# Optimization experiments

Hardware: AMD Instinct MI355X
Metric: run time of the kernel (lower is better)

The kernel has to match this reference:

```python
import jax, jax.numpy as jnp
import numpy as np

NUM_IMAGE_PATCHES = 4096
HIDDEN = 1536
NUM_HEADS = 12
HEAD_DIM = HIDDEN // NUM_HEADS  # 128
MLP_HIDDEN = 4 * HIDDEN  # 6144
TXT_LEN = 256
L_X = TXT_LEN + NUM_IMAGE_PATCHES  # 4352
NUM_CONCEPTS = 20
L_C = NUM_CONCEPTS + NUM_IMAGE_PATCHES  # 4116


def setup_inputs() -> dict:
    key = jax.random.key(0)
    ks = jax.random.split(key, 10)
    B = 1
    f = lambda k, s, sc=1.0: jax.random.normal(k, s, dtype=jnp.float32) * sc
    return {
        "x": f(ks[0], (B, L_X, HIDDEN)),
        "concepts": f(ks[1], (B, NUM_CONCEPTS, HIDDEN)),
        "vec": f(ks[2], (B, HIDDEN)),
        "pe": f(ks[3], (1, 1, L_X, HEAD_DIM // 2, 2, 2)),
        "concept_pe": f(ks[4], (1, 1, L_C, HEAD_DIM // 2, 2, 2)),
        # linear1: hidden -> 3*hidden + mlp_hidden (torch Linear: y = x @ W.T + b)
        "w1": f(ks[5], (3 * HIDDEN + MLP_HIDDEN, HIDDEN), 0.02),
        "b1": jnp.zeros((3 * HIDDEN + MLP_HIDDEN,), jnp.float32),
        # linear2: hidden + mlp_hidden -> hidden
        "w2": f(ks[6], (HIDDEN, HIDDEN + MLP_HIDDEN), 0.02),
        "b2": jnp.zeros((HIDDEN,), jnp.float32),
        # QKNorm learned RMSNorm scales (per head_dim)
        "q_scale": jnp.ones((HEAD_DIM,), jnp.float32),
        "k_scale": jnp.ones((HEAD_DIM,), jnp.float32),
        # Modulation(double=False): silu(vec) -> 3*hidden (shift, scale, gate)
        "mod_w": f(ks[7], (3 * HIDDEN, HIDDEN), 0.02),
        "mod_b": jnp.zeros((3 * HIDDEN,), jnp.float32),
    }


def _layernorm(x):  # elementwise_affine=False, eps=1e-6
    mu = x.mean(-1, keepdims=True)
    var = ((x - mu) ** 2).mean(-1, keepdims=True)
    return (x - mu) * jax.lax.rsqrt(var + 1e-6)


def _rmsnorm(x, scale):  # FLUX RMSNorm with learned scale
    return x * jax.lax.rsqrt((x * x).mean(-1, keepdims=True) + 1e-6) * scale


def _apply_rope(t, pe):
    # t: [B,H,L,D]; pe: [1,1,L,D/2,2,2]
    ts = t.reshape(*t.shape[:-1], -1, 1, 2)  # [B,H,L,D/2,1,2]
    out = pe[..., 0] * ts[..., 0] + pe[..., 1] * ts[..., 1]  # [B,H,L,D/2,2]
    return out.reshape(t.shape)


def _attention(q, k, v, pe):
    q = _apply_rope(q, pe)
    k = _apply_rope(k, pe)
    scale = jnp.asarray(1.0 / np.sqrt(q.shape[-1]), q.dtype)
    logits = jnp.einsum("bhqd,bhkd->bhqk", q, k) * scale
    a = jax.nn.softmax(logits, axis=-1)
    o = jnp.einsum("bhqk,bhkd->bhqd", a, v)
    B, H, L, D = o.shape
    return o.transpose(0, 2, 1, 3).reshape(B, L, H * D)  # B L (H D)


def reference(x, concepts, vec, pe, concept_pe, w1, b1, w2, b2,
              q_scale, k_scale, mod_w, mod_b):
    H = HIDDEN
    # Modulation: lin(silu(vec))[:, None].chunk(3) -> shift, scale, gate
    m = jax.nn.silu(vec) @ mod_w.T + mod_b
    shift, scale, gate = [t[:, None, :] for t in jnp.split(m, 3, axis=-1)]

    def block(inp, pe_in):
        xm = (1.0 + scale) * _layernorm(inp) + shift
        h = xm @ w1.T + b1
        qkv, mlp = h[..., : 3 * H], h[..., 3 * H:]
        B, L = inp.shape[0], inp.shape[1]
        # 'B L (K H D) -> K B H L D'
        qkv = qkv.reshape(B, L, 3, NUM_HEADS, HEAD_DIM).transpose(2, 0, 3, 1, 4)
        q, k, v = qkv[0], qkv[1], qkv[2]
        q = _rmsnorm(q, q_scale)
        k = _rmsnorm(k, k_scale)
        attn = _attention(q, k, v, pe_in)
        return jnp.concatenate([attn, jax.nn.gelu(mlp, approximate=True)], axis=2) @ w2.T + b2

    output = block(x, pe)

    img = x[:, -NUM_IMAGE_PATCHES:]
    img_concept_x = jnp.concatenate([concepts, img], axis=1)
    output_img_concept = block(img_concept_x, concept_pe)
    concept_output = output_img_concept[:, :-NUM_IMAGE_PATCHES]

    return (x + gate * output, concepts + gate * concept_output)
```

## Files before the change

kernel.cpp:

```cpp
#include <hip/hip_runtime.h>
#include <cstdint>
#include <cstddef>

typedef float        f32x4  __attribute__((ext_vector_type(4)));
typedef __bf16       bf16x8 __attribute__((ext_vector_type(8)));
typedef unsigned int u32x4  __attribute__((ext_vector_type(4)));
typedef unsigned int u32x2  __attribute__((ext_vector_type(2)));

static constexpr int HID   = 1536;
static constexpr int NHEAD = 12;
static constexpr int HD    = 128;
static constexpr int NQKV  = 10752;
static constexpr int CATK  = 7680;
static constexpr int LX    = 4352;
static constexpr int LC2   = 4116;
static constexpr int NCON  = 20;

static constexpr float QSCL = 0.08838834764831845f * 1.4426950408889634f;
static constexpr float SHIFT = 24.0f;

static constexpr size_t OFF_MVEC = 0;
static constexpr size_t OFF_W1B  = 18432;
static constexpr size_t OFF_W2B  = OFF_W1B  + 33030144ull;
static constexpr size_t OFF_XM1  = OFF_W2B  + 23592960ull;
static constexpr size_t OFF_QH1  = OFF_XM1;
static constexpr size_t OFF_QKV1 = OFF_XM1  + 13369344ull;
static constexpr size_t OFF_KH1  = OFF_QKV1 + 26738688ull;
static constexpr size_t OFF_VH1  = OFF_KH1  + 13369344ull;
static constexpr size_t OFF_CAT1 = OFF_VH1  + 13369344ull;
static constexpr size_t OFF_XM2  = OFF_CAT1;
static constexpr size_t OFF_QKV2 = OFF_XM2  + 196608ull;
static constexpr size_t OFF_VH2S = OFF_QKV2 + 196608ull;
static constexpr size_t OFF_QH2  = OFF_VH2S + 98304ull;
static constexpr size_t OFF_KH2  = OFF_QH2  + 196608ull;
static constexpr size_t OFF_CAT2 = OFF_KH2  + 12644352ull;

__device__ __forceinline__ void gload_lds16(const void* g, void* l)
{
  __builtin_amdgcn_global_load_lds(
      (const __attribute__((address_space(1))) unsigned int*)g,
      (__attribute__((address_space(3))) unsigned int*)l, 16, 0, 0);
}

#define PHASE_BAR() asm volatile("s_barrier" ::: "memory")


__global__ __launch_bounds__(256) void f2b_kernel(const float* __restrict__ in,
                                                  __bf16* __restrict__ out, int n4)
{
  int i = blockIdx.x * 256 + threadIdx.x;
  if (i >= n4) return;
  f32x4 v = *((const f32x4*)in + i);
  union { __bf16 h[4]; u32x2 u; } cv;
  cv.h[0] = (__bf16)v[0]; cv.h[1] = (__bf16)v[1];
  cv.h[2] = (__bf16)v[2]; cv.h[3] = (__bf16)v[3];
  *((u32x2*)out + i) = cv.u;
}

__global__ __launch_bounds__(256) void mod_kernel(const float* __restrict__ vec,
                                                  const float* __restrict__ mod_w,
                                                  const float* __restrict__ mod_b,
                                                  float* __restrict__ m)
{
  int o = blockIdx.x * 4 + (threadIdx.x >> 6);
  int lane = threadIdx.x & 63;
  float s = 0.0f;
  for (int k = lane; k < HID; k += 64) {
    float v = vec[k];
    float sv = v / (1.0f + expf(-v));
    s += sv * mod_w[(size_t)o * HID + k];
  }
  #pragma unroll
  for (int msk = 32; msk; msk >>= 1) s += __shfl_xor(s, msk);
  if (lane == 0) m[o] = s + mod_b[o];
}

__device__ __forceinline__ float block_sum256(float v, float* red)
{
  #pragma unroll
  for (int msk = 32; msk; msk >>= 1) v += __shfl_xor(v, msk);
  int w = threadIdx.x >> 6;
  if ((threadIdx.x & 63) == 0) red[w] = v;
  __syncthreads();
  float s = red[0] + red[1] + red[2] + red[3];
  __syncthreads();
  return s;
}

__global__ __launch_bounds__(256) void ln_mod_kernel(const float* __restrict__ x,
                                                     const float* __restrict__ mvec,
                                                     __bf16* __restrict__ out)
{
  __shared__ float red[4];
  size_t row = blockIdx.x;
  const float* xr = x + row * HID;
  float v[6]; float s = 0.0f;
  #pragma unroll
  for (int i = 0; i < 6; i++) { v[i] = xr[threadIdx.x + i * 256]; s += v[i]; }
  float mu = block_sum256(s, red) * (1.0f / HID);
  float s2 = 0.0f;
  #pragma unroll
  for (int i = 0; i < 6; i++) { float d = v[i] - mu; s2 += d * d; }
  float var = block_sum256(s2, red) * (1.0f / HID);
  float rinv = rsqrtf(var + 1e-6f);
  #pragma unroll
  for (int i = 0; i < 6; i++) {
    int h = threadIdx.x + i * 256;
    float xm = (v[i] - mu) * rinv;
    xm = (1.0f + mvec[HID + h]) * xm + mvec[h];
    out[row * HID + h] = (__bf16)xm;
  }
}

template<int MODE>
__global__ __launch_bounds__(512, 2) void gemm256(const __bf16* __restrict__ A,
                                                  const __bf16* __restrict__ B,
                                                  int M, int K,
                                                  const float* __restrict__ bias,
                                                  __bf16* __restrict__ qkv_out,
                                                  __bf16* __restrict__ cat_out,
                                                  __bf16* __restrict__ vh_out, int vkeys,
                                                  const float* __restrict__ res,
                                                  const float* __restrict__ gate,
                                                  float* __restrict__ out)
{
  const int tid = threadIdx.x;
  const int lane = tid & 63, wave = tid >> 6;
  const int quad = lane >> 4, l16 = lane & 15;
  const int wmh = wave >> 2;
  const int wnq = wave & 3;
  const int m0 = blockIdx.y * 256, n0 = blockIdx.x * 256;
  const int swz = (l16 & 4) ? 16 : 0;

  __shared__ __bf16 As[2][256][64];
  __shared__ __bf16 Bs[2][256][64];

  const f32x4 fzero = {0.0f, 0.0f, 0.0f, 0.0f};
  f32x4 acc[8][4];
  #pragma unroll
  for (int i = 0; i < 8; i++)
    #pragma unroll
    for (int j = 0; j < 4; j++) acc[i][j] = fzero;

  const int srow = lane >> 3;
  const int scol = ((lane & 7) * 8) ^ ((lane & 32) ? 16 : 0);
  const __bf16* Ag = A + (size_t)(m0 + wave * 32 + srow) * K + scol;
  const __bf16* Bg = B + (size_t)(n0 + wave * 32 + srow) * K + scol;

  auto stageA = [&](int buf, int k) {
    #pragma unroll
    for (int j = 0; j < 4; j++)
      gload_lds16(Ag + (size_t)(j * 8) * K + k, &As[buf][wave * 32 + j * 8][0]);
  };
  auto stageB = [&](int buf, int k) {
    #pragma unroll
    for (int j = 0; j < 4; j++)
      gload_lds16(Bg + (size_t)(j * 8) * K + k, &Bs[buf][wave * 32 + j * 8][0]);
  };

  const int NT = K >> 6;
  stageB(0, 0);  stageA(0, 0);
  stageB(1, 64); stageA(1, 64);
  asm volatile("s_waitcnt vmcnt(8)" ::: "memory");
  PHASE_BAR();

  for (int t = 0; t < NT; ++t) {
    const int b = t & 1;
    const int kn = (t + 2) << 6;
    bf16x8 aM[4][2], bN0[2][2], bN1[2][2];

    #pragma unroll
    for (int f = 0; f < 4; f++)
      #pragma unroll
      for (int kk = 0; kk < 2; kk++)
        aM[f][kk] = *(const bf16x8*)&As[b][wmh * 128 + f * 16 + l16][(kk * 32 + quad * 8) ^ swz];
    #pragma unroll
    for (int g = 0; g < 2; g++)
      #pragma unroll
      for (int kk = 0; kk < 2; kk++)
        bN0[g][kk] = *(const bf16x8*)&Bs[b][wnq * 64 + g * 16 + l16][(kk * 32 + quad * 8) ^ swz];
    PHASE_BAR();
    __builtin_amdgcn_s_setprio(1);
    #pragma unroll
    for (int f = 0; f < 4; f++)
      #pragma unroll
      for (int g = 0; g < 2; g++)
        #pragma unroll
        for (int kk = 0; kk < 2; kk++)
          acc[f][g] = __builtin_amdgcn_mfma_f32_16x16x32_bf16(aM[f][kk], bN0[g][kk], acc[f][g], 0, 0, 0);
    __builtin_amdgcn_s_setprio(0);
    PHASE_BAR();

    #pragma unroll
    for (int g = 0; g < 2; g++)
      #pragma unroll
      for (int kk = 0; kk < 2; kk++)
        bN1[g][kk] = *(const bf16x8*)&Bs[b][wnq * 64 + 32 + g * 16 + l16][(kk * 32 + quad * 8) ^ swz];
    PHASE_BAR();
    __builtin_amdgcn_s_setprio(1);
    #pragma unroll
    for (int f = 0; f < 4; f++)
      #pragma unroll
      for (int g = 0; g < 2; g++)
        #pragma unroll
        for (int kk = 0; kk < 2; kk++)
          acc[f][2 + g] = __builtin_amdgcn_mfma_f32_16x16x32_bf16(aM[f][kk], bN1[g][kk], acc[f][2 + g], 0, 0, 0);
    __builtin_amdgcn_s_setprio(0);
    PHASE_BAR();

    #pragma unroll
    for (int f = 0; f < 4; f++)
      #pragma unroll
      for (int kk = 0; kk < 2; kk++)
        aM[f][kk] = *(const bf16x8*)&As[b][wmh * 128 + 64 + f * 16 + l16][(kk * 32 + quad * 8) ^ swz];
    if (t + 2 < NT) stageB(b, kn);
    PHASE_BAR();
    __builtin_amdgcn_s_setprio(1);
    #pragma unroll
    for (int f = 0; f < 4; f++)
      #pragma unroll
      for (int g = 0; g < 2; g++)
        #pragma unroll
        for (int kk = 0; kk < 2; kk++)
          acc[4 + f][2 + g] = __builtin_amdgcn_mfma_f32_16x16x32_bf16(aM[f][kk], bN1[g][kk], acc[4 + f][2 + g], 0, 0, 0);
    __builtin_amdgcn_s_setprio(0);
    PHASE_BAR();

    if (t + 2 < NT) stageA(b, kn);
    PHASE_BAR();
    __builtin_amdgcn_s_setprio(1);
    #pragma unroll
    for (int f = 0; f < 4; f++)
      #pragma unroll
      for (int g = 0; g < 2; g++)
        #pragma unroll
        for (int kk = 0; kk < 2; kk++)
          acc[4 + f][g] = __builtin_amdgcn_mfma_f32_16x16x32_bf16(aM[f][kk], bN0[g][kk], acc[4 + f][g], 0, 0, 0);
    __builtin_amdgcn_s_setprio(0);
    if (t + 1 < NT) {
      if (t + 2 < NT) asm volatile("s_waitcnt vmcnt(8)" ::: "memory");
      else            asm volatile("s_waitcnt vmcnt(0)" ::: "memory");
    }
    PHASE_BAR();
  }

  #pragma unroll
  for (int mf = 0; mf < 8; mf++) {
    #pragma unroll
    for (int r = 0; r < 4; r++) {
      int gm = m0 + wmh * 128 + mf * 16 + quad * 4 + r;
      if (gm >= M) continue;
      #pragma unroll
      for (int nf = 0; nf < 4; nf++) {
        int gn = n0 + wnq * 64 + nf * 16 + l16;
        float v = acc[mf][nf][r] + bias[gn];
        if constexpr (MODE == 0) {
          if (gn < 3072) {
            qkv_out[(size_t)gm * 3072 + gn] = (__bf16)v;
          } else if (gn < 4608) {
            vh_out[(size_t)(gn - 3072) * vkeys + gm] = (__bf16)v;
          } else {
            float g = 0.5f * v * (1.0f + tanhf(0.7978845608028654f * (v + 0.044715f * v * v * v)));
            cat_out[(size_t)gm * CATK + (gn - 3072)] = (__bf16)g;
          }
        } else {
          out[(size_t)gm * HID + gn] = res[(size_t)gm * HID + gn] + gate[gn] * v;
        }
      }
    }
  }
}

template<int MODE>
__global__ __launch_bounds__(256) void gemm_bt(const __bf16* __restrict__ A,
                                               const __bf16* __restrict__ B,
                                               int M, int K,
                                               const float* __restrict__ bias,
                                               __bf16* __restrict__ qkv_out,
                                               __bf16* __restrict__ cat_out,
                                               __bf16* __restrict__ vh_out, int vkeys,
                                               const float* __restrict__ res,
                                               const float* __restrict__ gate,
                                               float* __restrict__ out)
{
  const int tid = threadIdx.x;
  const int lane = tid & 63, wave = tid >> 6;
  const int quad = lane >> 4, l16 = lane & 15;
  const int m0 = blockIdx.y * 128, n0 = blockIdx.x * 128;
  const int wm = (wave & 1) * 64, wn = (wave >> 1) * 64;

  __shared__ __bf16 As[128][64];
  __shared__ __bf16 Bs[128][64];

  const f32x4 fzero = {0.0f, 0.0f, 0.0f, 0.0f};
  f32x4 acc[4][4];
  #pragma unroll
  for (int i = 0; i < 4; i++)
    #pragma unroll
    for (int j = 0; j < 4; j++) acc[i][j] = fzero;

  const int srow = lane >> 3;
  const int scol = (lane & 7) * 8;
  const int rbase = wave * 32 + srow;
  const __bf16* Ab = A + (size_t)(m0 + rbase) * K + scol;
  const __bf16* Bb = B + (size_t)(n0 + rbase) * K + scol;

  for (int k0 = 0; k0 < K; k0 += 64) {
    __syncthreads();
    #pragma unroll
    for (int j = 0; j < 4; j++) {
      gload_lds16(Ab + (size_t)(j * 8) * K + k0, &As[wave * 32 + j * 8][0]);
      gload_lds16(Bb + (size_t)(j * 8) * K + k0, &Bs[wave * 32 + j * 8][0]);
    }
    __syncthreads();
    #pragma unroll
    for (int kk = 0; kk < 64; kk += 32) {
      bf16x8 af[4], bfr[4];
      #pragma unroll
      for (int i = 0; i < 4; i++) af[i]  = *(const bf16x8*)&As[wm + i * 16 + l16][kk + quad * 8];
      #pragma unroll
      for (int j = 0; j < 4; j++) bfr[j] = *(const bf16x8*)&Bs[wn + j * 16 + l16][kk + quad * 8];
      #pragma unroll
      for (int i = 0; i < 4; i++)
        #pragma unroll
        for (int j = 0; j < 4; j++)
          acc[i][j] = __builtin_amdgcn_mfma_f32_16x16x32_bf16(af[i], bfr[j], acc[i][j], 0, 0, 0);
    }
  }

  #pragma unroll
  for (int i = 0; i < 4; i++) {
    #pragma unroll
    for (int r = 0; r < 4; r++) {
      int gm = m0 + wm + i * 16 + quad * 4 + r;
      if (gm >= M) continue;
      #pragma unroll
      for (int j = 0; j < 4; j++) {
        int gn = n0 + wn + j * 16 + l16;
        float v = acc[i][j][r] + bias[gn];
        if constexpr (MODE == 0) {
          if (gn < 3072) {
            qkv_out[(size_t)gm * 3072 + gn] = (__bf16)v;
          } else if (gn < 4608) {
            vh_out[(size_t)(gn - 3072) * vkeys + gm] = (__bf16)v;
          } else {
            float g = 0.5f * v * (1.0f + tanhf(0.7978845608028654f * (v + 0.044715f * v * v * v)));
            cat_out[(size_t)gm * CATK + (gn - 3072)] = (__bf16)g;
          }
        } else {
          out[(size_t)gm * HID + gn] = res[(size_t)gm * HID + gn] + gate[gn] * v;
        }
      }
    }
  }
}

__global__ __launch_bounds__(256) void qk_prep(const __bf16* __restrict__ src0, int rows0,
                                               const __bf16* __restrict__ src1, int off1,
                                               int total_rows, int q_rows,
                                               const float* __restrict__ pe,
                                               const float* __restrict__ qscale,
                                               const float* __restrict__ kscale,
                                               __bf16* __restrict__ qh, int q_stride,
                                               __bf16* __restrict__ kh, int k_stride)
{
  int wid = blockIdx.x * 4 + (threadIdx.x >> 6);
  int lane = threadIdx.x & 63;
  int r = wid / NHEAD, h = wid - (wid / NHEAD) * NHEAD;
  if (r >= total_rows) return;
  const __bf16* src = (r < rows0) ? (src0 + (size_t)r * 3072)
                                  : (src1 + (size_t)(r + off1) * 3072);
  const float* pep = pe + ((size_t)r * 64 + lane) * 4;
  float e00 = pep[0], e01 = pep[1], e10 = pep[2], e11 = pep[3];

  {
    const __bf16* p = src + HID + h * HD + 2 * lane;
    float a = (float)p[0], b = (float)p[1];
    float ss = a * a + b * b;
    #pragma unroll
    for (int msk = 32; msk; msk >>= 1) ss += __shfl_xor(ss, msk);
    float rinv = rsqrtf(ss * (1.0f / HD) + 1e-6f);
    a *= rinv * kscale[2 * lane]; b *= rinv * kscale[2 * lane + 1];
    float ra = e00 * a + e01 * b, rb = e10 * a + e11 * b;
    __bf16* o = kh + ((size_t)h * k_stride + r) * HD + 2 * lane;
    o[0] = (__bf16)ra; o[1] = (__bf16)rb;
  }
  if (r < q_rows) {
    const __bf16* p = src + h * HD + 2 * lane;
    float a = (float)p[0], b = (float)p[1];
    float ss = a * a + b * b;
    #pragma unroll
    for (int msk = 32; msk; msk >>= 1) ss += __shfl_xor(ss, msk);
    float rinv = rsqrtf(ss * (1.0f / HD) + 1e-6f);
    a *= rinv * qscale[2 * lane]; b *= rinv * qscale[2 * lane + 1];
    float ra = (e00 * a + e01 * b) * QSCL, rb = (e10 * a + e11 * b) * QSCL;
    __bf16* o = qh + ((size_t)h * q_stride + r) * HD + 2 * lane;
    o[0] = (__bf16)ra; o[1] = (__bf16)rb;
  }
}

template<int GEN>
__global__ __launch_bounds__(512, 4) void attn_kernel(const __bf16* __restrict__ qh,
                                                      const __bf16* __restrict__ kh,
                                                      const __bf16* __restrict__ vA, int vA_stride,
                                                      const __bf16* __restrict__ vB, int vB_stride,
                                                      int v_boff, int v_split,
                                                      int Lq, int Lk, int q_stride, int k_stride,
                                                      int nqt,
                                                      __bf16* __restrict__ cat_out)
{
  const int tid = threadIdx.x, lane = tid & 63, wave = tid >> 6;
  const int quad = lane >> 4, l16 = lane & 15;
  const int qsub = wave >> 1, kg = wave & 1;

  int bid = blockIdx.x;
  if constexpr (GEN == 0) {
    int nb = gridDim.x;
    if ((nb & 7) == 0) {
      int per = nb >> 3;
      bid = (bid & 7) * per + (bid >> 3);
    }
  }
  const int head = bid / nqt, qt = bid - head * nqt;
  const int q0 = qt * 64 + qsub * 16;

  __shared__ __align__(16) unsigned char lds_raw[46080];
  __bf16 (*Ks)[136]     = (__bf16(*)[136])(lds_raw);
  __bf16 (*Vt)[72]      = (__bf16(*)[72])(lds_raw + 17408);
  __bf16 (*Ps)[16][40]  = (__bf16(*)[16][40])(lds_raw + 35840);
  float*  Of            = (float*)lds_raw;
  float*  Lf            = (float*)(lds_raw + 35840);

  const f32x4 fzero = {0.0f, 0.0f, 0.0f, 0.0f};
  const u32x4 uzero = {0, 0, 0, 0};

  bf16x8 ones;
  #pragma unroll
  for (int e = 0; e < 8; e++) ones[e] = (__bf16)1.0f;

  bf16x8 qf[4];
  {
    int qrow = q0 + l16;
    if (GEN == 0 || qrow < Lq) {
      const __bf16* qp = qh + ((size_t)head * q_stride + qrow) * HD + quad * 8;
      #pragma unroll
      for (int c = 0; c < 4; c++) qf[c] = *(const bf16x8*)(qp + c * 32);
    } else {
      #pragma unroll
      for (int c = 0; c < 4; c++) qf[c] = __builtin_bit_cast(bf16x8, uzero);
    }
  }
  f32x4 o[8];
  #pragma unroll
  for (int d = 0; d < 8; d++) o[d] = fzero;
  f32x4 l_acc = fzero;

  const int krowA = tid >> 4, kcolA = (tid & 15) * 8;
  const int vdimA = tid >> 3, vkcA  = tid & 7;

  const __bf16* khb = kh + (size_t)head * k_stride * HD;
  const __bf16* vaB = vA + (size_t)head * HD * vA_stride;
  const __bf16* vbB = vB + (size_t)head * HD * vB_stride + v_boff;

  auto vload = [&](int dim, int kb) -> u32x4 {
    if constexpr (GEN == 0) {
      return *(const u32x4*)(vbB + (size_t)dim * vB_stride + kb);
    } else {
      u32x4 vd = uzero;
      if (kb < Lk) {
        if (kb + 8 <= v_split) {
          vd = *(const u32x4*)(vaB + (size_t)dim * vA_stride + kb);
        } else if (kb >= v_split && kb + 8 <= Lk) {
          vd = *(const u32x4*)(vbB + (size_t)dim * vB_stride + kb);
        } else {
          __bf16* ve = (__bf16*)&vd;
          #pragma unroll
          for (int e = 0; e < 8; e++) {
            int key = kb + e;
            if (key < Lk)
              ve[e] = (key < v_split) ? vaB[(size_t)dim * vA_stride + key]
                                      : vbB[(size_t)dim * vB_stride + key];
          }
        }
      }
      return vd;
    }
  };
  auto kload = [&](int kr, int col) -> u32x4 {
    if constexpr (GEN == 0) {
      return *(const u32x4*)(khb + (size_t)kr * HD + col);
    } else {
      return (kr < Lk) ? *(const u32x4*)(khb + (size_t)kr * HD + col) : uzero;
    }
  };

  u32x4 pk0, pk1, pv0, pv1;
  pk0 = kload(krowA, kcolA);
  pk1 = kload(krowA + 32, kcolA);
  pv0 = vload(vdimA, vkcA * 8);
  pv1 = vload(vdimA + 64, vkcA * 8);

  const int nkt = (Lk + 63) >> 6;
  for (int t = 0; t < nkt; ++t) {
    const int kt0 = t * 64;
    __syncthreads();
    *(u32x4*)&Ks[krowA][kcolA]      = pk0;
    *(u32x4*)&Ks[krowA + 32][kcolA] = pk1;
    *(u32x4*)&Vt[vdimA][vkcA * 8]      = pv0;
    *(u32x4*)&Vt[vdimA + 64][vkcA * 8] = pv1;
    if (t + 1 < nkt) {
      const int nt0 = kt0 + 64;
      pk0 = kload(nt0 + krowA, kcolA);
      pk1 = kload(nt0 + krowA + 32, kcolA);
      pv0 = vload(vdimA, nt0 + vkcA * 8);
      pv1 = vload(vdimA + 64, nt0 + vkcA * 8);
    }
    __syncthreads();

    f32x4 s[2];
    __builtin_amdgcn_s_setprio(1);
    #pragma unroll
    for (int nt = 0; nt < 2; nt++) {
      s[nt] = fzero;
      #pragma unroll
      for (int c = 0; c < 4; c++) {
        bf16x8 b = *(const bf16x8*)&Ks[kg * 32 + nt * 16 + l16][c * 32 + quad * 8];
        s[nt] = __builtin_amdgcn_mfma_f32_16x16x32_bf16(qf[c], b, s[nt], 0, 0, 0);
      }
      if constexpr (GEN != 0) {
        int kidx = kt0 + kg * 32 + nt * 16 + l16;
        if (kidx >= Lk) { s[nt][0] = -1e30f; s[nt][1] = -1e30f; s[nt][2] = -1e30f; s[nt][3] = -1e30f; }
      }
    }
    __builtin_amdgcn_s_setprio(0);

    #pragma unroll
    for (int r = 0; r < 4; r++) {
      int prow = quad * 4 + r;
      Ps[wave][prow][l16]      = (__bf16)exp2f(s[0][r] - SHIFT);
      Ps[wave][prow][16 + l16] = (__bf16)exp2f(s[1][r] - SHIFT);
    }

    bf16x8 pf = *(const bf16x8*)&Ps[wave][l16][quad * 8];
    __builtin_amdgcn_s_setprio(1);
    l_acc = __builtin_amdgcn_mfma_f32_16x16x32_bf16(pf, ones, l_acc, 0, 0, 0);
    #pragma unroll
    for (int dt = 0; dt < 8; dt++) {
      bf16x8 bv = *(const bf16x8*)&Vt[dt * 16 + l16][kg * 32 + quad * 8];
      o[dt] = __builtin_amdgcn_mfma_f32_16x16x32_bf16(pf, bv, o[dt], 0, 0, 0);
    }
    __builtin_amdgcn_s_setprio(0);
  }

  __syncthreads();
  if (l16 == 0) {
    #pragma unroll
    for (int r = 0; r < 4; r++) Lf[wave * 16 + quad * 4 + r] = l_acc[r];
  }
  __syncthreads();
  float inv_den[4];
  #pragma unroll
  for (int r = 0; r < 4; r++)
    inv_den[r] = 1.0f / (l_acc[r] + Lf[(wave ^ 1) * 16 + quad * 4 + r]);
  if (kg == 0) {
    #pragma unroll
    for (int d = 0; d < 8; d++)
      #pragma unroll
      for (int r = 0; r < 4; r++)
        Of[(size_t)(qsub * 16 + quad * 4 + r) * 132 + d * 16 + l16] = o[d][r];
  }
  __syncthreads();
  if (kg == 1) {
    #pragma unroll
    for (int r = 0; r < 4; r++) {
      int qrow = q0 + quad * 4 + r;
      if (qrow >= Lq) continue;
      #pragma unroll
      for (int d = 0; d < 8; d++) {
        float v = Of[(size_t)(qsub * 16 + quad * 4 + r) * 132 + d * 16 + l16] + o[d][r];
        cat_out[(size_t)qrow * CATK + head * HD + d * 16 + l16] = (__bf16)(v * inv_den[r]);
      }
    }
  }
}

extern "C" void kernel_launch(void* const* d_in, const int* in_sizes, int n_in,
                              void* d_out, int out_size, void* d_ws, size_t ws_size,
                              hipStream_t stream)
{
  const float* x   = (const float*)d_in[0];
  const float* con = (const float*)d_in[1];
  const float* vec = (const float*)d_in[2];
  const float* pe  = (const float*)d_in[3];
  const float* cpe = (const float*)d_in[4];
  const float* w1  = (const float*)d_in[5];
  const float* b1  = (const float*)d_in[6];
  const float* w2  = (const float*)d_in[7];
  const float* b2  = (const float*)d_in[8];
  const float* qsc = (const float*)d_in[9];
  const float* ksc = (const float*)d_in[10];
  const float* mw  = (const float*)d_in[11];
  const float* mb  = (const float*)d_in[12];
  float* out = (float*)d_out;

  char* ws = (char*)d_ws;
  float*  mvec = (float*)(ws + OFF_MVEC);
  __bf16* w1b  = (__bf16*)(ws + OFF_W1B);
  __bf16* w2b  = (__bf16*)(ws + OFF_W2B);
  __bf16* xm1  = (__bf16*)(ws + OFF_XM1);
  __bf16* qh1  = (__bf16*)(ws + OFF_QH1);
  __bf16* qkv1 = (__bf16*)(ws + OFF_QKV1);
  __bf16* kh1  = (__bf16*)(ws + OFF_KH1);
  __bf16* vh1  = (__bf16*)(ws + OFF_VH1);
  __bf16* cat1 = (__bf16*)(ws + OFF_CAT1);
  __bf16* xm2  = (__bf16*)(ws + OFF_XM2);
  __bf16* qkv2 = (__bf16*)(ws + OFF_QKV2);
  __bf16* vh2s = (__bf16*)(ws + OFF_VH2S);
  __bf16* qh2  = (__bf16*)(ws + OFF_QH2);
  __bf16* kh2  = (__bf16*)(ws + OFF_KH2);
  __bf16* cat2 = (__bf16*)(ws + OFF_CAT2);

  f2b_kernel<<<16128, 256, 0, stream>>>(w1, w1b, (NQKV * HID) / 4);
  f2b_kernel<<<11520, 256, 0, stream>>>(w2, w2b, (HID * CATK) / 4);
  mod_kernel<<<1152, 256, 0, stream>>>(vec, mw, mb, mvec);

  ln_mod_kernel<<<LX, 256, 0, stream>>>(x, mvec, xm1);
  gemm256<0><<<dim3(NQKV / 256, LX / 256), 512, 0, stream>>>(
      xm1, w1b, LX, HID, b1, qkv1, cat1, vh1, LX, nullptr, nullptr, nullptr);
  qk_prep<<<(LX * NHEAD) / 4, 256, 0, stream>>>(
      qkv1, LX, qkv1, 0, LX, LX, pe, qsc, ksc, qh1, LX, kh1, LX);
  attn_kernel<0><<<NHEAD * (LX / 64), 512, 0, stream>>>(
      qh1, kh1, vh1, LX, vh1, LX, 0, 0, LX, LX, LX, LX, LX / 64, cat1);
  gemm256<1><<<dim3(HID / 256, LX / 256), 512, 0, stream>>>(
      cat1, w2b, LX, CATK, b2, nullptr, nullptr, nullptr, 0, x, mvec + 3072, out);

  ln_mod_kernel<<<NCON, 256, 0, stream>>>(con, mvec, xm2);
  gemm_bt<0><<<dim3(NQKV / 128, 1), 256, 0, stream>>>(
      xm2, w1b, NCON, HID, b1, qkv2, cat2, vh2s, 32, nullptr, nullptr, nullptr);
  qk_prep<<<(LC2 * NHEAD + 3) / 4, 256, 0, stream>>>(
      qkv2, NCON, qkv1, 236, LC2, NCON, cpe, qsc, ksc, qh2, 64, kh2, LC2);
  attn_kernel<1><<<NHEAD, 512, 0, stream>>>(
      qh2, kh2, vh2s, 32, vh1, LX, 236, NCON, NCON, LC2, 64, LC2, 1, cat2);
  gemm_bt<1><<<dim3(HID / 128, 1), 256, 0, stream>>>(
      cat2, w2b, NCON, CATK, b2, nullptr, nullptr, nullptr, 0, con, mvec + 3072,
      out + (size_t)LX * HID);
}
```

Baseline: 1.319 ms.

## Split-K the second GEMM with atomic accumulation and switch to XOR row swizzle

The output projection GEMM (K=7680, only 6x17=102 tiles) now runs as a split-K over 5 slices along grid z. Each slice atomically adds gate*partial into the output, which the layernorm kernel pre-initialises with x + gate*b2. This is meant to fill the GPU with more blocks than the original tile grid provides, at the cost of float atomics, a non-deterministic summation order and extra output traffic. The LDS layout also changes from a 2-way swizzle to a full 8-way XOR row swizzle in both GEMM kernels, to reduce bank conflicts on fragment reads.

```diff
diff --git a/kernel.cpp b/kernel.cpp
--- a/kernel.cpp
+++ b/kernel.cpp
@@ -89,7 +89,9 @@
 
 __global__ __launch_bounds__(256) void ln_mod_kernel(const float* __restrict__ x,
                                                      const float* __restrict__ mvec,
-                                                     __bf16* __restrict__ out)
+                                                     __bf16* __restrict__ out,
+                                                     const float* __restrict__ b2,
+                                                     float* __restrict__ outp)
 {
   __shared__ float red[4];
   size_t row = blockIdx.x;
@@ -109,13 +111,14 @@
     float xm = (v[i] - mu) * rinv;
     xm = (1.0f + mvec[HID + h]) * xm + mvec[h];
     out[row * HID + h] = (__bf16)xm;
+    if (outp) outp[row * HID + h] = v[i] + mvec[3072 + h] * b2[h];
   }
 }
 
 template<int MODE>
 __global__ __launch_bounds__(512, 2) void gemm256(const __bf16* __restrict__ A,
                                                   const __bf16* __restrict__ B,
-                                                  int M, int K,
+                                                  int M, int K, int lda,
                                                   const float* __restrict__ bias,
                                                   __bf16* __restrict__ qkv_out,
                                                   __bf16* __restrict__ cat_out,
@@ -130,7 +133,8 @@
   const int wmh = wave >> 2;
   const int wnq = wave & 3;
   const int m0 = blockIdx.y * 256, n0 = blockIdx.x * 256;
-  const int swz = (l16 & 4) ? 16 : 0;
+  const int kstart = blockIdx.z * K;
+  const int rsw = l16 & 7;
 
   __shared__ __bf16 As[2][256][64];
   __shared__ __bf16 Bs[2][256][64];
@@ -143,19 +147,19 @@
     for (int j = 0; j < 4; j++) acc[i][j] = fzero;
 
   const int srow = lane >> 3;
-  const int scol = ((lane & 7) * 8) ^ ((lane & 32) ? 16 : 0);
-  const __bf16* Ag = A + (size_t)(m0 + wave * 32 + srow) * K + scol;
-  const __bf16* Bg = B + (size_t)(n0 + wave * 32 + srow) * K + scol;
+  const int scol = ((lane & 7) ^ srow) * 8;
+  const __bf16* Ag = A + (size_t)(m0 + wave * 32 + srow) * lda + kstart + scol;
+  const __bf16* Bg = B + (size_t)(n0 + wave * 32 + srow) * lda + kstart + scol;
 
   auto stageA = [&](int buf, int k) {
     #pragma unroll
     for (int j = 0; j < 4; j++)
-      gload_lds16(Ag + (size_t)(j * 8) * K + k, &As[buf][wave * 32 + j * 8][0]);
+      gload_lds16(Ag + (size_t)(j * 8) * lda + k, &As[buf][wave * 32 + j * 8][0]);
   };
   auto stageB = [&](int buf, int k) {
     #pragma unroll
     for (int j = 0; j < 4; j++)
-      gload_lds16(Bg + (size_t)(j * 8) * K + k, &Bs[buf][wave * 32 + j * 8][0]);
+      gload_lds16(Bg + (size_t)(j * 8) * lda + k, &Bs[buf][wave * 32 + j * 8][0]);
   };
 
   const int NT = K >> 6;
@@ -173,12 +177,12 @@
     for (int f = 0; f < 4; f++)
       #pragma unroll
       for (int kk = 0; kk < 2; kk++)
-        aM[f][kk] = *(const bf16x8*)&As[b][wmh * 128 + f * 16 + l16][(kk * 32 + quad * 8) ^ swz];
+        aM[f][kk] = *(const bf16x8*)&As[b][wmh * 128 + f * 16 + l16][((kk * 4 + quad) ^ rsw) * 8];
     #pragma unroll
     for (int g = 0; g < 2; g++)
       #pragma unroll
       for (int kk = 0; kk < 2; kk++)
-        bN0[g][kk] = *(const bf16x8*)&Bs[b][wnq * 64 + g * 16 + l16][(kk * 32 + quad * 8) ^ swz];
+        bN0[g][kk] = *(const bf16x8*)&Bs[b][wnq * 64 + g * 16 + l16][((kk * 4 + quad) ^ rsw) * 8];
     PHASE_BAR();
     __builtin_amdgcn_s_setprio(1);
     #pragma unroll
@@ -195,7 +199,7 @@
     for (int g = 0; g < 2; g++)
       #pragma unroll
       for (int kk = 0; kk < 2; kk++)
-        bN1[g][kk] = *(const bf16x8*)&Bs[b][wnq * 64 + 32 + g * 16 + l16][(kk * 32 + quad * 8) ^ swz];
+        bN1[g][kk] = *(const bf16x8*)&Bs[b][wnq * 64 + 32 + g * 16 + l16][((kk * 4 + quad) ^ rsw) * 8];
     PHASE_BAR();
     __builtin_amdgcn_s_setprio(1);
     #pragma unroll
@@ -212,7 +216,7 @@
     for (int f = 0; f < 4; f++)
       #pragma unroll
       for (int kk = 0; kk < 2; kk++)
-        aM[f][kk] = *(const bf16x8*)&As[b][wmh * 128 + 64 + f * 16 + l16][(kk * 32 + quad * 8) ^ swz];
+        aM[f][kk] = *(const bf16x8*)&As[b][wmh * 128 + 64 + f * 16 + l16][((kk * 4 + quad) ^ rsw) * 8];
     if (t + 2 < NT) stageB(b, kn);
     PHASE_BAR();
     __builtin_amdgcn_s_setprio(1);
@@ -253,8 +257,8 @@
       #pragma unroll
       for (int nf = 0; nf < 4; nf++) {
         int gn = n0 + wnq * 64 + nf * 16 + l16;
-        float v = acc[mf][nf][r] + bias[gn];
         if constexpr (MODE == 0) {
+          float v = acc[mf][nf][r] + bias[gn];
           if (gn < 3072) {
             qkv_out[(size_t)gm * 3072 + gn] = (__bf16)v;
           } else if (gn < 4608) {
@@ -263,8 +267,11 @@
             float g = 0.5f * v * (1.0f + tanhf(0.7978845608028654f * (v + 0.044715f * v * v * v)));
             cat_out[(size_t)gm * CATK + (gn - 3072)] = (__bf16)g;
           }
+        } else if constexpr (MODE == 1) {
+          float v = acc[mf][nf][r] + bias[gn];
+          out[(size_t)gm * HID + gn] = res[(size_t)gm * HID + gn] + gate[gn] * v;
         } else {
-          out[(size_t)gm * HID + gn] = res[(size_t)gm * HID + gn] + gate[gn] * v;
+          unsafeAtomicAdd(&out[(size_t)gm * HID + gn], gate[gn] * acc[mf][nf][r]);
         }
       }
     }
@@ -288,6 +295,7 @@
   const int quad = lane >> 4, l16 = lane & 15;
   const int m0 = blockIdx.y * 128, n0 = blockIdx.x * 128;
   const int wm = (wave & 1) * 64, wn = (wave >> 1) * 64;
+  const int rsw = l16 & 7;
 
   __shared__ __bf16 As[128][64];
   __shared__ __bf16 Bs[128][64];
@@ -300,7 +308,7 @@
     for (int j = 0; j < 4; j++) acc[i][j] = fzero;
 
   const int srow = lane >> 3;
-  const int scol = (lane & 7) * 8;
+  const int scol = ((lane & 7) ^ srow) * 8;
   const int rbase = wave * 32 + srow;
   const __bf16* Ab = A + (size_t)(m0 + rbase) * K + scol;
   const __bf16* Bb = B + (size_t)(n0 + rbase) * K + scol;
@@ -314,12 +322,12 @@
     }
     __syncthreads();
     #pragma unroll
-    for (int kk = 0; kk < 64; kk += 32) {
+    for (int kk = 0; kk < 2; kk++) {
       bf16x8 af[4], bfr[4];
       #pragma unroll
-      for (int i = 0; i < 4; i++) af[i]  = *(const bf16x8*)&As[wm + i * 16 + l16][kk + quad * 8];
-      #pragma unroll
-      for (int j = 0; j < 4; j++) bfr[j] = *(const bf16x8*)&Bs[wn + j * 16 + l16][kk + quad * 8];
+      for (int i = 0; i < 4; i++) af[i]  = *(const bf16x8*)&As[wm + i * 16 + l16][((kk * 4 + quad) ^ rsw) * 8];
+      #pragma unroll
+      for (int j = 0; j < 4; j++) bfr[j] = *(const bf16x8*)&Bs[wn + j * 16 + l16][((kk * 4 + quad) ^ rsw) * 8];
       #pragma unroll
       for (int i = 0; i < 4; i++)
         #pragma unroll
@@ -624,17 +632,18 @@
   f2b_kernel<<<11520, 256, 0, stream>>>(w2, w2b, (HID * CATK) / 4);
   mod_kernel<<<1152, 256, 0, stream>>>(vec, mw, mb, mvec);
 
-  ln_mod_kernel<<<LX, 256, 0, stream>>>(x, mvec, xm1);
+  ln_mod_kernel<<<LX, 256, 0, stream>>>(x, mvec, xm1, b2, out);
   gemm256<0><<<dim3(NQKV / 256, LX / 256), 512, 0, stream>>>(
-      xm1, w1b, LX, HID, b1, qkv1, cat1, vh1, LX, nullptr, nullptr, nullptr);
+      xm1, w1b, LX, HID, HID, b1, qkv1, cat1, vh1, LX, nullptr, nullptr, nullptr);
   qk_prep<<<(LX * NHEAD) / 4, 256, 0, stream>>>(
       qkv1, LX, qkv1, 0, LX, LX, pe, qsc, ksc, qh1, LX, kh1, LX);
   attn_kernel<0><<<NHEAD * (LX / 64), 512, 0, stream>>>(
       qh1, kh1, vh1, LX, vh1, LX, 0, 0, LX, LX, LX, LX, LX / 64, cat1);
-  gemm256<1><<<dim3(HID / 256, LX / 256), 512, 0, stream>>>(
-      cat1, w2b, LX, CATK, b2, nullptr, nullptr, nullptr, 0, x, mvec + 3072, out);
-
-  ln_mod_kernel<<<NCON, 256, 0, stream>>>(con, mvec, xm2);
+  gemm256<2><<<dim3(HID / 256, LX / 256, 5), 512, 0, stream>>>(
+      cat1, w2b, LX, CATK / 5, CATK, b2, nullptr, nullptr, nullptr, 0,
+      nullptr, mvec + 3072, out);
+
+  ln_mod_kernel<<<NCON, 256, 0, stream>>>(con, mvec, xm2, nullptr, nullptr);
   gemm_bt<0><<<dim3(NQKV / 128, 1), 256, 0, stream>>>(
       xm2, w1b, NCON, HID, b1, qkv2, cat2, vh2s, 32, nullptr, nullptr, nullptr);
   qk_prep<<<(LC2 * NHEAD + 3) / 4, 256, 0, stream>>>(
```

Measured after the change: 1.244 ms. 1.06x faster.
